# Performance work log

Measured on AMD Instinct MI355X. Metric: run time of the kernel, lower is better.

The kernel has to match this reference:

```python
import jax, jax.numpy as jnp
import numpy as np

B, T = 64, 2048
VOCAB, H, OUT = 32000, 256, 256


def setup_inputs() -> dict:
    key = jax.random.key(0)
    ks = jax.random.split(key, 6)
    x = jax.random.randint(ks[0], (B, T), 0, VOCAB, dtype=jnp.int32)
    embed = jax.random.normal(ks[1], (VOCAB, H), dtype=jnp.float32) * 0.02
    # torch Linear(h+h, h): weight [h, 2h]; we store transposed [2h, h]
    W_fc = jax.random.normal(ks[2], (2 * H, H), dtype=jnp.float32) * (1.0 / np.sqrt(2 * H))
    b_fc = jax.random.normal(ks[3], (H,), dtype=jnp.float32) * 0.01
    W_out = jax.random.normal(ks[4], (H, OUT), dtype=jnp.float32) * (1.0 / np.sqrt(H))
    b_out = jax.random.normal(ks[5], (OUT,), dtype=jnp.float32) * 0.01
    return {"x": x, "embed": embed, "W_fc": W_fc, "b_fc": b_fc, "W_out": W_out, "b_out": b_out}


def reference(x, embed, W_fc, b_fc, W_out, b_out):
    # SimpleRNN.forward_bptt: h_t = tanh(fc(concat([embed(x_t), h_{t-1}])))
    # concat-linear split: fc([e, h]) = e @ Wx + h @ Wh + b
    h_dim = embed.shape[1]
    Wx, Wh = W_fc[:h_dim], W_fc[h_dim:]
    xe = embed[x]                                   # [B, T, H] gather
    xproj = jnp.einsum('bth,hk->btk', xe, Wx) + b_fc  # precompute input projection

    def step(h, xp_t):
        h_new = jnp.tanh(xp_t + h @ Wh)
        return h_new, h_new

    h0 = jnp.zeros((x.shape[0], h_dim), dtype=embed.dtype)
    h_last, hs = jax.lax.scan(step, h0, jnp.swapaxes(xproj, 0, 1))  # hs: [T, B, H]
    hs = jnp.swapaxes(hs, 0, 1)                     # [B, T, H] = stack(hs[1:], dim=1)
    out = h_last @ W_out + b_out                    # [B, OUT]
    return out, hs
```

## Files before the change

kernel.cpp:

```cpp
#include <hip/hip_runtime.h>

#define RNN_T 2048
#define RNN_B 64
#define RNN_H 256

__global__ __launch_bounds__(256)
void xproj_kernel(const int* __restrict__ x, const float* __restrict__ embed,
                  const float* __restrict__ Wfc, const float* __restrict__ bfc,
                  float* __restrict__ hsb) {
    __shared__ int ixs[64];
    __shared__ __align__(16) float A[64][260];
    const int tid = threadIdx.x;
    const long rb0 = (long)blockIdx.x * 64;

    if (tid < 64) ixs[tid] = x[rb0 + tid];
    __syncthreads();

    {
        const int r = tid >> 2, q = tid & 3;
        const float* erow = embed + (long)ixs[r] * RNN_H;
        #pragma unroll
        for (int i = 0; i < 16; ++i) {
            const int c = q * 64 + i * 4;
            *(float4*)&A[r][c] = *(const float4*)(erow + c);
        }
    }
    __syncthreads();

    const int tj = tid & 31, tr = tid >> 5;
    const int r0 = tr * 8, j0 = tj * 4, j1 = 128 + tj * 4;

    float acc[8][8];
    #pragma unroll
    for (int i = 0; i < 8; ++i)
        #pragma unroll
        for (int c = 0; c < 8; ++c) acc[i][c] = 0.f;

    for (int k4 = 0; k4 < 64; ++k4) {
        float4 a[8];
        #pragma unroll
        for (int i = 0; i < 8; ++i) a[i] = *(const float4*)&A[r0 + i][k4 * 4];
        #pragma unroll
        for (int kk = 0; kk < 4; ++kk) {
            const int k = k4 * 4 + kk;
            const float4 wa = *(const float4*)(Wfc + (long)k * RNN_H + j0);
            const float4 wb = *(const float4*)(Wfc + (long)k * RNN_H + j1);
            #pragma unroll
            for (int i = 0; i < 8; ++i) {
                const float av = reinterpret_cast<const float*>(&a[i])[kk];
                acc[i][0] = fmaf(av, wa.x, acc[i][0]);
                acc[i][1] = fmaf(av, wa.y, acc[i][1]);
                acc[i][2] = fmaf(av, wa.z, acc[i][2]);
                acc[i][3] = fmaf(av, wa.w, acc[i][3]);
                acc[i][4] = fmaf(av, wb.x, acc[i][4]);
                acc[i][5] = fmaf(av, wb.y, acc[i][5]);
                acc[i][6] = fmaf(av, wb.z, acc[i][6]);
                acc[i][7] = fmaf(av, wb.w, acc[i][7]);
            }
        }
    }

    const float4 ba = *(const float4*)(bfc + j0);
    const float4 bb = *(const float4*)(bfc + j1);
    #pragma unroll
    for (int i = 0; i < 8; ++i) {
        const long row = rb0 + r0 + i;
        float4 o1 = make_float4(acc[i][0] + ba.x, acc[i][1] + ba.y,
                                acc[i][2] + ba.z, acc[i][3] + ba.w);
        float4 o2 = make_float4(acc[i][4] + bb.x, acc[i][5] + bb.y,
                                acc[i][6] + bb.z, acc[i][7] + bb.w);
        *(float4*)(hsb + row * RNN_H + j0) = o1;
        *(float4*)(hsb + row * RNN_H + j1) = o2;
    }
}

__global__ __launch_bounds__(512, 2)
void rnn_scan_kernel(const float* __restrict__ Wfc, const float* __restrict__ Wout,
                     const float* __restrict__ bout, float* __restrict__ out,
                     float* __restrict__ hsb) {
    __shared__ __align__(16) float h[RNN_H];
    __shared__ float part[4 * RNN_H];
    const int tid = threadIdx.x;
    const int b = blockIdx.x;
    const int jj = tid & 127, ks = tid >> 7;

    const float* Wh = Wfc + RNN_H * RNN_H;
    float w0[64], w1[64];
    #pragma unroll
    for (int i = 0; i < 64; ++i) {
        w0[i] = Wh[(long)(ks * 64 + i) * RNN_H + jj];
        w1[i] = Wh[(long)(ks * 64 + i) * RNN_H + jj + 128];
    }

    if (tid < RNN_H) h[tid] = 0.f;

    float* xpb = hsb + (long)b * RNN_T * RNN_H;
    float xr = 0.f, xrn = 0.f;
    if (tid < RNN_H) xr = xpb[tid];
    __syncthreads();

    const float4* h4 = (const float4*)h;
    for (int t = 0; t < RNN_T; ++t) {
        if (tid < RNN_H && t + 1 < RNN_T) xrn = xpb[(long)(t + 1) * RNN_H + tid];

        float acc0 = 0.f, acc1 = 0.f;
        #pragma unroll
        for (int i4 = 0; i4 < 16; ++i4) {
            const float4 hv = h4[ks * 16 + i4];
            acc0 = fmaf(hv.x, w0[i4 * 4 + 0], acc0);
            acc0 = fmaf(hv.y, w0[i4 * 4 + 1], acc0);
            acc0 = fmaf(hv.z, w0[i4 * 4 + 2], acc0);
            acc0 = fmaf(hv.w, w0[i4 * 4 + 3], acc0);
            acc1 = fmaf(hv.x, w1[i4 * 4 + 0], acc1);
            acc1 = fmaf(hv.y, w1[i4 * 4 + 1], acc1);
            acc1 = fmaf(hv.z, w1[i4 * 4 + 2], acc1);
            acc1 = fmaf(hv.w, w1[i4 * 4 + 3], acc1);
        }
        part[ks * RNN_H + jj]       = acc0;
        part[ks * RNN_H + jj + 128] = acc1;
        __syncthreads();

        if (tid < RNN_H) {
            const float s = part[tid] + part[RNN_H + tid] + part[2 * RNN_H + tid]
                          + part[3 * RNN_H + tid] + xr;
            const float e = __expf(2.f * s);
            const float hn = 1.f - 2.f / (e + 1.f);
            h[tid] = hn;
            xpb[(long)t * RNN_H + tid] = hn;
            xr = xrn;
        }
        __syncthreads();
    }

    if (tid < RNN_H) {
        float a0 = 0.f, a1 = 0.f, a2 = 0.f, a3 = 0.f;
        for (int k = 0; k < RNN_H; k += 4) {
            a0 = fmaf(h[k + 0], Wout[(long)(k + 0) * RNN_H + tid], a0);
            a1 = fmaf(h[k + 1], Wout[(long)(k + 1) * RNN_H + tid], a1);
            a2 = fmaf(h[k + 2], Wout[(long)(k + 2) * RNN_H + tid], a2);
            a3 = fmaf(h[k + 3], Wout[(long)(k + 3) * RNN_H + tid], a3);
        }
        out[(long)b * RNN_H + tid] = a0 + a1 + a2 + a3 + bout[tid];
    }
}

extern "C" void kernel_launch(void* const* d_in, const int* in_sizes, int n_in,
                              void* d_out, int out_size, void* d_ws, size_t ws_size,
                              hipStream_t stream) {
    const int*   x     = (const int*)d_in[0];
    const float* embed = (const float*)d_in[1];
    const float* Wfc   = (const float*)d_in[2];
    const float* bfc   = (const float*)d_in[3];
    const float* Wout  = (const float*)d_in[4];
    const float* bout  = (const float*)d_in[5];

    float* out = (float*)d_out;
    float* hsb = out + RNN_B * RNN_H;

    xproj_kernel<<<(RNN_B * RNN_T) / 64, 256, 0, stream>>>(x, embed, Wfc, bfc, hsb);
    rnn_scan_kernel<<<RNN_B, 512, 0, stream>>>(Wfc, Wout, bout, out, hsb);
}
```

Measured before the change: 1.638 ms.

## Restructure RNN scan with DPP reductions, double-buffered h and one barrier per step

Each thread now owns 4 output columns over a 32-wide k slice, with the weights held as packed float2 registers. The 8 partial sums for a column are reduced with cross-lane DPP instead of a shared-memory partial array. The hidden state is double-buffered in shared memory with padded rows, which drops one of the two barriers per timestep, and the xproj prefetch is pushed two steps ahead. This targets the serial per-step latency of the recurrence (shared-memory traffic, barriers, reduction) but depends on a correct DPP lane pattern and on the register-pinning asm not causing spills.

```diff
diff --git a/kernel.cpp b/kernel.cpp
--- a/kernel.cpp
+++ b/kernel.cpp
@@ -3,6 +3,9 @@
 #define RNN_T 2048
 #define RNN_B 64
 #define RNN_H 256
+#define KBLK 36
+
+typedef float v2f __attribute__((ext_vector_type(2)));
 
 __global__ __launch_bounds__(256)
 void xproj_kernel(const int* __restrict__ x, const float* __restrict__ embed,
@@ -74,71 +77,118 @@
     }
 }
 
+__device__ __forceinline__ float red8_dpp(float x) {
+    int v = __float_as_int(x);
+    x += __int_as_float(__builtin_amdgcn_update_dpp(0, v, 0xB1, 0xf, 0xf, true));
+    v = __float_as_int(x);
+    x += __int_as_float(__builtin_amdgcn_update_dpp(0, v, 0x4E, 0xf, 0xf, true));
+    v = __float_as_int(x);
+    x += __int_as_float(__builtin_amdgcn_update_dpp(0, v, 0x141, 0xf, 0xf, true));
+    return x;
+}
+
+__device__ __forceinline__ v2f lo2(const float4 v) { return (v2f){v.x, v.y}; }
+__device__ __forceinline__ v2f hi2(const float4 v) { return (v2f){v.z, v.w}; }
+
 __global__ __launch_bounds__(512, 2)
 void rnn_scan_kernel(const float* __restrict__ Wfc, const float* __restrict__ Wout,
                      const float* __restrict__ bout, float* __restrict__ out,
                      float* __restrict__ hsb) {
-    __shared__ __align__(16) float h[RNN_H];
-    __shared__ float part[4 * RNN_H];
+    __shared__ __align__(16) float hA[8 * KBLK];
+    __shared__ __align__(16) float hB[8 * KBLK];
     const int tid = threadIdx.x;
     const int b = blockIdx.x;
-    const int jj = tid & 127, ks = tid >> 7;
+    const int w = tid >> 6, l = tid & 63;
+    const int cg = w * 8 + (l >> 3);
+    const int kg = l & 7;
+    const int c0 = cg * 4;
+    const int k0 = kg * 32;
 
     const float* Wh = Wfc + RNN_H * RNN_H;
-    float w0[64], w1[64];
-    #pragma unroll
-    for (int i = 0; i < 64; ++i) {
-        w0[i] = Wh[(long)(ks * 64 + i) * RNN_H + jj];
-        w1[i] = Wh[(long)(ks * 64 + i) * RNN_H + jj + 128];
-    }
-
-    if (tid < RNN_H) h[tid] = 0.f;
+    v2f wv[4][16];
+    #pragma unroll
+    for (int m = 0; m < 16; ++m) {
+        const long kb = (long)(k0 + 2 * m) * RNN_H;
+        #pragma unroll
+        for (int c = 0; c < 4; ++c) {
+            v2f t;
+            t.x = Wh[kb + c0 + c];
+            t.y = Wh[kb + RNN_H + c0 + c];
+            wv[c][m] = t;
+        }
+    }
+    #pragma unroll
+    for (int m = 0; m < 16; ++m)
+        asm volatile("" : "+v"(wv[0][m]), "+v"(wv[1][m]), "+v"(wv[2][m]), "+v"(wv[3][m]));
+
+    if (tid < 8 * KBLK) { hA[tid] = 0.f; }
 
     float* xpb = hsb + (long)b * RNN_T * RNN_H;
-    float xr = 0.f, xrn = 0.f;
-    if (tid < RNN_H) xr = xpb[tid];
+    const bool wr = (kg < 4);
+    const int jcol = c0 + (kg & 3);
+    const int widx = (jcol >> 5) * KBLK + (jcol & 31);
+    float* xw = xpb + jcol;
+    const float* xpf = xpb + jcol + 2 * RNN_H;
+    const float* xend = xpb + (long)RNN_T * RNN_H;
+
+    float xr = 0.f, xn = 0.f;
+    if (wr) { xr = xpb[jcol]; xn = xpb[RNN_H + jcol]; }
     __syncthreads();
 
-    const float4* h4 = (const float4*)h;
-    for (int t = 0; t < RNN_T; ++t) {
-        if (tid < RNN_H && t + 1 < RNN_T) xrn = xpb[(long)(t + 1) * RNN_H + tid];
-
-        float acc0 = 0.f, acc1 = 0.f;
-        #pragma unroll
-        for (int i4 = 0; i4 < 16; ++i4) {
-            const float4 hv = h4[ks * 16 + i4];
-            acc0 = fmaf(hv.x, w0[i4 * 4 + 0], acc0);
-            acc0 = fmaf(hv.y, w0[i4 * 4 + 1], acc0);
-            acc0 = fmaf(hv.z, w0[i4 * 4 + 2], acc0);
-            acc0 = fmaf(hv.w, w0[i4 * 4 + 3], acc0);
-            acc1 = fmaf(hv.x, w1[i4 * 4 + 0], acc1);
-            acc1 = fmaf(hv.y, w1[i4 * 4 + 1], acc1);
-            acc1 = fmaf(hv.z, w1[i4 * 4 + 2], acc1);
-            acc1 = fmaf(hv.w, w1[i4 * 4 + 3], acc1);
-        }
-        part[ks * RNN_H + jj]       = acc0;
-        part[ks * RNN_H + jj + 128] = acc1;
-        __syncthreads();
-
-        if (tid < RNN_H) {
-            const float s = part[tid] + part[RNN_H + tid] + part[2 * RNN_H + tid]
-                          + part[3 * RNN_H + tid] + xr;
-            const float e = __expf(2.f * s);
-            const float hn = 1.f - 2.f / (e + 1.f);
-            h[tid] = hn;
-            xpb[(long)t * RNN_H + tid] = hn;
-            xr = xrn;
-        }
-        __syncthreads();
-    }
+    const float4* rdA = (const float4*)(hA + kg * KBLK);
+    const float4* rdB = (const float4*)(hB + kg * KBLK);
+
+#define RNN_STEP(RD, WDST)                                                  \
+    {                                                                       \
+        float xf = 0.f;                                                     \
+        if (wr && xpf < xend) xf = *xpf;                                    \
+        xpf += RNN_H;                                                       \
+        const float4 q0 = RD[0], q1 = RD[1], q2 = RD[2], q3 = RD[3];        \
+        const float4 q4 = RD[4], q5 = RD[5], q6 = RD[6], q7 = RD[7];        \
+        v2f a0 = {0.f,0.f}, a1 = {0.f,0.f}, a2 = {0.f,0.f}, a3 = {0.f,0.f}; \
+        const v2f hp[16] = { lo2(q0), hi2(q0), lo2(q1), hi2(q1),            \
+                             lo2(q2), hi2(q2), lo2(q3), hi2(q3),            \
+                             lo2(q4), hi2(q4), lo2(q5), hi2(q5),            \
+                             lo2(q6), hi2(q6), lo2(q7), hi2(q7) };          \
+        _Pragma("unroll")                                                   \
+        for (int m = 0; m < 16; ++m) {                                      \
+            a0 = __builtin_elementwise_fma(hp[m], wv[0][m], a0);            \
+            a1 = __builtin_elementwise_fma(hp[m], wv[1][m], a1);            \
+            a2 = __builtin_elementwise_fma(hp[m], wv[2][m], a2);            \
+            a3 = __builtin_elementwise_fma(hp[m], wv[3][m], a3);            \
+        }                                                                   \
+        const float r0 = red8_dpp(a0.x + a0.y);                             \
+        const float r1 = red8_dpp(a1.x + a1.y);                             \
+        const float r2 = red8_dpp(a2.x + a2.y);                             \
+        const float r3 = red8_dpp(a3.x + a3.y);                             \
+        if (wr) {                                                           \
+            const float sv = (kg == 0) ? r0 : (kg == 1) ? r1                \
+                           : (kg == 2) ? r2 : r3;                           \
+            const float vsum = sv + xr;                                     \
+            const float e = __expf(2.f * vsum);                             \
+            const float hn = 1.f - 2.f * __builtin_amdgcn_rcpf(e + 1.f);    \
+            WDST[widx] = hn;                                                \
+            *xw = hn;                                                       \
+            xr = xn; xn = xf;                                               \
+        }                                                                   \
+        xw += RNN_H;                                                        \
+        __syncthreads();                                                    \
+    }
+
+    for (int t = 0; t < RNN_T; t += 2) {
+        RNN_STEP(rdA, hB);
+        RNN_STEP(rdB, hA);
+    }
+#undef RNN_STEP
 
     if (tid < RNN_H) {
         float a0 = 0.f, a1 = 0.f, a2 = 0.f, a3 = 0.f;
         for (int k = 0; k < RNN_H; k += 4) {
-            a0 = fmaf(h[k + 0], Wout[(long)(k + 0) * RNN_H + tid], a0);
-            a1 = fmaf(h[k + 1], Wout[(long)(k + 1) * RNN_H + tid], a1);
-            a2 = fmaf(h[k + 2], Wout[(long)(k + 2) * RNN_H + tid], a2);
-            a3 = fmaf(h[k + 3], Wout[(long)(k + 3) * RNN_H + tid], a3);
+            const int kb = (k >> 5) * KBLK + (k & 31);
+            a0 = fmaf(hA[kb + 0], Wout[(long)(k + 0) * RNN_H + tid], a0);
+            a1 = fmaf(hA[kb + 1], Wout[(long)(k + 1) * RNN_H + tid], a1);
+            a2 = fmaf(hA[kb + 2], Wout[(long)(k + 2) * RNN_H + tid], a2);
+            a3 = fmaf(hA[kb + 3], Wout[(long)(k + 3) * RNN_H + tid], a3);
         }
         out[(long)b * RNN_H + tid] = a0 + a1 + a2 + a3 + bout[tid];
     }
```

Result: faster. 1.464 ms (-10.6%).

## Rewrite RNN scan with f16 MFMA over 16-batch tiles and double-buffered LDS

Applied to the files above, without the earlier changes.

The recurrent scan now runs 4 workgroups, each handling 16 batch rows. The hidden-to-hidden product uses f16 MFMA 16x16x32, with Wh held in registers as f16 fragments and h double-buffered in swizzled LDS, so each step needs a single barrier. The cross-thread partial-sum reduction goes away and tanh uses a fast reciprocal. The output projection moves into a separate kernel. This trades the 64-block parallelism for fewer, denser blocks and lowers precision to f16 for h and Wh, which may drift over 2048 steps.

```diff
diff --git a/kernel.cpp b/kernel.cpp
--- a/kernel.cpp
+++ b/kernel.cpp
@@ -3,6 +3,11 @@
 #define RNN_T 2048
 #define RNN_B 64
 #define RNN_H 256
+
+typedef _Float16 f16;
+typedef _Float16 f16x4 __attribute__((ext_vector_type(4)));
+typedef _Float16 f16x8 __attribute__((ext_vector_type(8)));
+typedef float f32x4 __attribute__((ext_vector_type(4)));
 
 __global__ __launch_bounds__(256)
 void xproj_kernel(const int* __restrict__ x, const float* __restrict__ embed,
@@ -74,74 +79,128 @@
     }
 }
 
-__global__ __launch_bounds__(512, 2)
-void rnn_scan_kernel(const float* __restrict__ Wfc, const float* __restrict__ Wout,
-                     const float* __restrict__ bout, float* __restrict__ out,
-                     float* __restrict__ hsb) {
-    __shared__ __align__(16) float h[RNN_H];
-    __shared__ float part[4 * RNN_H];
+#define LDS_BARRIER() asm volatile("s_waitcnt lgkmcnt(0)\n\ts_barrier" ::: "memory")
+
+#define TANH1(d, s) { const float _e = __expf(2.f * (s));                     \
+                      d = 1.f - 2.f * __builtin_amdgcn_rcpf(_e + 1.f); }
+
+__global__ __launch_bounds__(256, 1)
+void rnn_scan_mfma(const float* __restrict__ Wfc, float* __restrict__ hsb) {
+    __shared__ __align__(16) f16 hA[16 * RNN_H];
+    __shared__ __align__(16) f16 hB[16 * RNN_H];
     const int tid = threadIdx.x;
-    const int b = blockIdx.x;
-    const int jj = tid & 127, ks = tid >> 7;
+    const int wg  = blockIdx.x;
+    const int wv = tid >> 6, l = tid & 63;
+    const int m = l & 15, g = l >> 4;
+    const int swz = m * 16;
 
     const float* Wh = Wfc + RNN_H * RNN_H;
-    float w0[64], w1[64];
+    f16x8 af[4][8];
     #pragma unroll
-    for (int i = 0; i < 64; ++i) {
-        w0[i] = Wh[(long)(ks * 64 + i) * RNN_H + jj];
-        w1[i] = Wh[(long)(ks * 64 + i) * RNN_H + jj + 128];
-    }
-
-    if (tid < RNN_H) h[tid] = 0.f;
-
-    float* xpb = hsb + (long)b * RNN_T * RNN_H;
-    float xr = 0.f, xrn = 0.f;
-    if (tid < RNN_H) xr = xpb[tid];
+    for (int nt = 0; nt < 4; ++nt) {
+        const int n = 64 * wv + nt * 16 + m;
+        #pragma unroll
+        for (int kt = 0; kt < 8; ++kt) {
+            #pragma unroll
+            for (int i = 0; i < 8; ++i) {
+                const int k = kt * 32 + g * 8 + i;
+                af[nt][kt][i] = (f16)Wh[k * RNN_H + n];
+            }
+        }
+    }
+
+    {
+        int* z = (int*)hA;
+        #pragma unroll
+        for (int i = 0; i < 8; ++i) z[tid + 256 * i] = 0;
+    }
+
+    float* const xbase = hsb + (long)(wg * 16 + m) * RNN_T * RNN_H;
+    const int n00 = 64 * wv + g * 4;
+
+    f32x4 xr0 = *(const f32x4*)(xbase + n00 +  0);
+    f32x4 xr1 = *(const f32x4*)(xbase + n00 + 16);
+    f32x4 xr2 = *(const f32x4*)(xbase + n00 + 32);
+    f32x4 xr3 = *(const f32x4*)(xbase + n00 + 48);
+    f32x4 xn0 = *(const f32x4*)(xbase + RNN_H + n00 +  0);
+    f32x4 xn1 = *(const f32x4*)(xbase + RNN_H + n00 + 16);
+    f32x4 xn2 = *(const f32x4*)(xbase + RNN_H + n00 + 32);
+    f32x4 xn3 = *(const f32x4*)(xbase + RNN_H + n00 + 48);
+
+    const float* xpf  = xbase + 2 * RNN_H;
+    const float* xend = xbase + (long)RNN_T * RNN_H;
+    float*       xw   = xbase;
+
+    char* const hAc = (char*)hA;
+    char* const hBc = (char*)hB;
+
     __syncthreads();
 
-    const float4* h4 = (const float4*)h;
-    for (int t = 0; t < RNN_T; ++t) {
-        if (tid < RNN_H && t + 1 < RNN_T) xrn = xpb[(long)(t + 1) * RNN_H + tid];
-
-        float acc0 = 0.f, acc1 = 0.f;
-        #pragma unroll
-        for (int i4 = 0; i4 < 16; ++i4) {
-            const float4 hv = h4[ks * 16 + i4];
-            acc0 = fmaf(hv.x, w0[i4 * 4 + 0], acc0);
-            acc0 = fmaf(hv.y, w0[i4 * 4 + 1], acc0);
-            acc0 = fmaf(hv.z, w0[i4 * 4 + 2], acc0);
-            acc0 = fmaf(hv.w, w0[i4 * 4 + 3], acc0);
-            acc1 = fmaf(hv.x, w1[i4 * 4 + 0], acc1);
-            acc1 = fmaf(hv.y, w1[i4 * 4 + 1], acc1);
-            acc1 = fmaf(hv.z, w1[i4 * 4 + 2], acc1);
-            acc1 = fmaf(hv.w, w1[i4 * 4 + 3], acc1);
-        }
-        part[ks * RNN_H + jj]       = acc0;
-        part[ks * RNN_H + jj + 128] = acc1;
-        __syncthreads();
-
-        if (tid < RNN_H) {
-            const float s = part[tid] + part[RNN_H + tid] + part[2 * RNN_H + tid]
-                          + part[3 * RNN_H + tid] + xr;
-            const float e = __expf(2.f * s);
-            const float hn = 1.f - 2.f / (e + 1.f);
-            h[tid] = hn;
-            xpb[(long)t * RNN_H + tid] = hn;
-            xr = xrn;
-        }
-        __syncthreads();
-    }
-
-    if (tid < RNN_H) {
-        float a0 = 0.f, a1 = 0.f, a2 = 0.f, a3 = 0.f;
-        for (int k = 0; k < RNN_H; k += 4) {
-            a0 = fmaf(h[k + 0], Wout[(long)(k + 0) * RNN_H + tid], a0);
-            a1 = fmaf(h[k + 1], Wout[(long)(k + 1) * RNN_H + tid], a1);
-            a2 = fmaf(h[k + 2], Wout[(long)(k + 2) * RNN_H + tid], a2);
-            a3 = fmaf(h[k + 3], Wout[(long)(k + 3) * RNN_H + tid], a3);
-        }
-        out[(long)b * RNN_H + tid] = a0 + a1 + a2 + a3 + bout[tid];
-    }
+#define RNN_STEP(RC, WC)                                                      \
+    {                                                                         \
+        f32x4 ac0 = {0,0,0,0}, ac1 = {0,0,0,0};                               \
+        f32x4 ac2 = {0,0,0,0}, ac3 = {0,0,0,0};                               \
+        _Pragma("unroll")                                                     \
+        for (int kt = 0; kt < 8; ++kt) {                                      \
+            const f16x8 bf = *(const f16x8*)(RC + m * 512 +                   \
+                                             ((kt * 64 + g * 16) ^ swz));     \
+            ac0 = __builtin_amdgcn_mfma_f32_16x16x32_f16(af[0][kt], bf, ac0, 0, 0, 0); \
+            ac1 = __builtin_amdgcn_mfma_f32_16x16x32_f16(af[1][kt], bf, ac1, 0, 0, 0); \
+            ac2 = __builtin_amdgcn_mfma_f32_16x16x32_f16(af[2][kt], bf, ac2, 0, 0, 0); \
+            ac3 = __builtin_amdgcn_mfma_f32_16x16x32_f16(af[3][kt], bf, ac3, 0, 0, 0); \
+        }                                                                     \
+        const f32x4 s0 = ac0 + xr0, s1 = ac1 + xr1;                           \
+        const f32x4 s2 = ac2 + xr2, s3 = ac3 + xr3;                           \
+        f32x4 h0, h1, h2, h3;                                                 \
+        TANH1(h0.x, s0.x) TANH1(h0.y, s0.y) TANH1(h0.z, s0.z) TANH1(h0.w, s0.w) \
+        TANH1(h1.x, s1.x) TANH1(h1.y, s1.y) TANH1(h1.z, s1.z) TANH1(h1.w, s1.w) \
+        TANH1(h2.x, s2.x) TANH1(h2.y, s2.y) TANH1(h2.z, s2.z) TANH1(h2.w, s2.w) \
+        TANH1(h3.x, s3.x) TANH1(h3.y, s3.y) TANH1(h3.z, s3.z) TANH1(h3.w, s3.w) \
+        f16x4 p0, p1, p2, p3;                                                 \
+        p0.x=(f16)h0.x; p0.y=(f16)h0.y; p0.z=(f16)h0.z; p0.w=(f16)h0.w;       \
+        p1.x=(f16)h1.x; p1.y=(f16)h1.y; p1.z=(f16)h1.z; p1.w=(f16)h1.w;       \
+        p2.x=(f16)h2.x; p2.y=(f16)h2.y; p2.z=(f16)h2.z; p2.w=(f16)h2.w;       \
+        p3.x=(f16)h3.x; p3.y=(f16)h3.y; p3.z=(f16)h3.z; p3.w=(f16)h3.w;       \
+        *(f16x4*)(WC + m * 512 + (((n00 +  0) * 2) ^ swz)) = p0;              \
+        *(f16x4*)(WC + m * 512 + (((n00 + 16) * 2) ^ swz)) = p1;              \
+        *(f16x4*)(WC + m * 512 + (((n00 + 32) * 2) ^ swz)) = p2;              \
+        *(f16x4*)(WC + m * 512 + (((n00 + 48) * 2) ^ swz)) = p3;              \
+        *(f32x4*)(xw + n00 +  0) = h0;                                        \
+        *(f32x4*)(xw + n00 + 16) = h1;                                        \
+        *(f32x4*)(xw + n00 + 32) = h2;                                        \
+        *(f32x4*)(xw + n00 + 48) = h3;                                        \
+        xw += RNN_H;                                                          \
+        xr0 = xn0; xr1 = xn1; xr2 = xn2; xr3 = xn3;                           \
+        if (xpf < xend) {                                                     \
+            xn0 = *(const f32x4*)(xpf + n00 +  0);                            \
+            xn1 = *(const f32x4*)(xpf + n00 + 16);                            \
+            xn2 = *(const f32x4*)(xpf + n00 + 32);                            \
+            xn3 = *(const f32x4*)(xpf + n00 + 48);                            \
+        }                                                                     \
+        xpf += RNN_H;                                                         \
+        LDS_BARRIER();                                                        \
+    }
+
+    for (int t = 0; t < RNN_T; t += 2) {
+        RNN_STEP(hAc, hBc);
+        RNN_STEP(hBc, hAc);
+    }
+#undef RNN_STEP
+}
+
+__global__ __launch_bounds__(256)
+void out_kernel(const float* __restrict__ hsb, const float* __restrict__ Wout,
+                const float* __restrict__ bout, float* __restrict__ out) {
+    const int b = blockIdx.x, n = threadIdx.x;
+    const float* hl = hsb + ((long)b * RNN_T + (RNN_T - 1)) * RNN_H;
+    float a0 = 0.f, a1 = 0.f, a2 = 0.f, a3 = 0.f;
+    for (int k = 0; k < RNN_H; k += 4) {
+        a0 = fmaf(hl[k + 0], Wout[(long)(k + 0) * RNN_H + n], a0);
+        a1 = fmaf(hl[k + 1], Wout[(long)(k + 1) * RNN_H + n], a1);
+        a2 = fmaf(hl[k + 2], Wout[(long)(k + 2) * RNN_H + n], a2);
+        a3 = fmaf(hl[k + 3], Wout[(long)(k + 3) * RNN_H + n], a3);
+    }
+    out[(long)b * RNN_H + n] = a0 + a1 + a2 + a3 + bout[n];
 }
 
 extern "C" void kernel_launch(void* const* d_in, const int* in_sizes, int n_in,
@@ -158,5 +217,6 @@
     float* hsb = out + RNN_B * RNN_H;
 
     xproj_kernel<<<(RNN_B * RNN_T) / 64, 256, 0, stream>>>(x, embed, Wfc, bfc, hsb);
-    rnn_scan_kernel<<<RNN_B, 512, 0, stream>>>(Wfc, Wout, bout, out, hsb);
-}
+    rnn_scan_mfma<<<4, 256, 0, stream>>>(Wfc, hsb);
+    out_kernel<<<RNN_B, 256, 0, stream>>>(hsb, Wout, bout, out);
+}
```

After: 2.466 ms. 50.5% more time.
